# Optimization experiments

Hardware: AMD Instinct MI355X
Metric: run time of the kernel (lower is better)

Reference implementation:

```python
import jax, jax.numpy as jnp
import numpy as np

B, S, L, H, D = 32, 512, 8, 1024, 64  # batch, max seq len, max span, hidden, MLP width


def setup_inputs() -> dict:
    key = jax.random.key(0)
    ks = jax.random.split(key, 8)
    return {
        "hidden": jax.random.normal(ks[0], (B, S, H), jnp.float32),
        "seq_lengths": jax.random.randint(ks[1], (B,), S // 2, S + 1),
        "term_weight": jax.random.normal(ks[2], (H,), jnp.float32),
        "W1": jax.random.normal(ks[3], (H, D), jnp.float32) * 0.02,
        "b1": jnp.zeros((D,), jnp.float32),
        "W2": jax.random.normal(ks[4], (D, 1), jnp.float32) * 0.02,
        "b2": jnp.zeros((1,), jnp.float32),
        "Ws": jax.random.normal(ks[5], (H, 1), jnp.float32) * 0.02,
        "bs": jnp.zeros((1,), jnp.float32),
    }


def reference(hidden, seq_lengths, term_weight, W1, b1, W2, b2, Ws, bs):
    """Batched candidate-span TermAttention + span scoring.

    For each sentence b (true length seq_lengths[b]) and start s, spans of
    nominal length l+1 (l in 0..L-1) cover positions s..s+l clipped to the
    sentence end, exactly as get_candidate_span_pairs/get_span_hiddens.
    TermAttention: softmax over MLP((h * w)) within the span, weighted sum,
    then spanEmb2Score linear -> scalar per span.
    """
    Bn, Sn, Hn = hidden.shape
    j = jnp.arange(L)
    s = jnp.arange(Sn)
    pos = jnp.minimum(s[:, None] + j[None, :], Sn - 1)          # [S,L] clipped gather idx
    g = hidden[:, pos]                                           # [B,S,L,H] span positions
    # per-position attention logit (independent of span length)
    e = (jax.nn.relu((g * term_weight) @ W1 + b1) @ W2 + b2)[..., 0]  # [B,S,L]
    # valid_pos[b,s,jp]: position s+jp is inside sentence b
    valid_pos = (s[:, None] + j[None, :])[None] < seq_lengths[:, None, None]  # [B,S,L]
    # m[b,s,l,jp]: position jp belongs to span of length l+1 and is in-sentence
    tri = j[:, None] >= j[None, :]                               # [L,L] jp <= l
    m = valid_pos[:, :, None, :] & tri[None, None]               # [B,S,L,L]
    logits = jnp.where(m, e[:, :, None, :], -1e9)
    a = jax.nn.softmax(logits, axis=-1) * m                      # [B,S,L,L]
    emb = jnp.einsum('bslj,bsjh->bslh', a, g)                    # span embeddings
    scores = (emb @ Ws + bs)[..., 0]                             # [B,S,L]
    valid_span = s[None, :, None] < seq_lengths[:, None, None]
    return jnp.where(valid_span, scores, 0.0)
```

## Files before the change

kernel.cpp:

```cpp
#include <hip/hip_runtime.h>
#include <hip/hip_bf16.h>

#define BB 32
#define SS 512
#define LL 8
#define HH 1024
#define DD 64

#define BM 32
#define BK 32
#define APAD 40

typedef __attribute__((ext_vector_type(8))) short bf16x8;
typedef __attribute__((ext_vector_type(4))) float f32x4;

__device__ __forceinline__ unsigned short f2bf(float x) {
    unsigned int u = __float_as_uint(x);
    u += 0x7FFFu + ((u >> 16) & 1u);
    return (unsigned short)(u >> 16);
}

__global__ void k_prep(const float* __restrict__ W1,
                       const float* __restrict__ tw,
                       unsigned short* __restrict__ W1pT) {
    int i = blockIdx.x * 256 + threadIdx.x;
    int h = i >> 6;
    int d = i & 63;
    float val = tw[h] * W1[i];
    W1pT[d * HH + h] = f2bf(val);
}

__global__ __launch_bounds__(256) void k_main(
        const float* __restrict__ hidden,
        const unsigned short* __restrict__ W1pT,
        const float* __restrict__ b1,
        const float* __restrict__ W2,
        const float* __restrict__ b2,
        const float* __restrict__ Ws,
        float* __restrict__ e1,
        float* __restrict__ vout) {
    __shared__ unsigned short Alds[BM * APAD];
    __shared__ unsigned short Blds[DD * APAD];
    __shared__ float eplds[4][BM];

    const int tid = threadIdx.x;
    const int row0 = blockIdx.x * BM;

    const int ln   = tid & 63;
    const int wv   = tid >> 6;
    const int ln15 = ln & 15;
    const int quad = ln >> 4;

    const int ar  = tid >> 3;
    const int ako = (tid & 7) * 4;
    const int bd  = tid >> 2;
    const int bko = (tid & 3) * 8;

    f32x4 acc0 = {0.f, 0.f, 0.f, 0.f};
    f32x4 acc1 = {0.f, 0.f, 0.f, 0.f};
    float vp = 0.f;

    const float* arow = hidden + (size_t)(row0 + ar) * HH + ako;
    const unsigned short* brow = W1pT + (size_t)bd * HH + bko;

    for (int k0 = 0; k0 < HH; k0 += BK) {
        float4 h4 = *(const float4*)(arow + k0);
        float4 w4 = *(const float4*)(Ws + k0 + ako);
        vp += h4.x * w4.x + h4.y * w4.y + h4.z * w4.z + h4.w * w4.w;
        ushort4 a4;
        a4.x = f2bf(h4.x); a4.y = f2bf(h4.y); a4.z = f2bf(h4.z); a4.w = f2bf(h4.w);
        *(ushort4*)&Alds[ar * APAD + ako] = a4;
        *(uint4*)&Blds[bd * APAD + bko] = *(const uint4*)(brow + k0);
        __syncthreads();

        bf16x8 bfrag = *(const bf16x8*)&Blds[(wv * 16 + ln15) * APAD + quad * 8];
        bf16x8 af0   = *(const bf16x8*)&Alds[(ln15) * APAD + quad * 8];
        bf16x8 af1   = *(const bf16x8*)&Alds[(16 + ln15) * APAD + quad * 8];
        acc0 = __builtin_amdgcn_mfma_f32_16x16x32_bf16(af0, bfrag, acc0, 0, 0, 0);
        acc1 = __builtin_amdgcn_mfma_f32_16x16x32_bf16(af1, bfrag, acc1, 0, 0, 0);
        __syncthreads();
    }

    vp += __shfl_xor(vp, 1);
    vp += __shfl_xor(vp, 2);
    vp += __shfl_xor(vp, 4);
    if ((tid & 7) == 0) vout[row0 + (tid >> 3)] = vp;

    const int col = wv * 16 + ln15;
    const float b1c = b1[col];
    const float w2c = W2[col];
    float ep[8];
#pragma unroll
    for (int reg = 0; reg < 4; reg++) {
        float x0 = acc0[reg] + b1c;
        float x1 = acc1[reg] + b1c;
        ep[reg]     = fmaxf(x0, 0.f) * w2c;
        ep[4 + reg] = fmaxf(x1, 0.f) * w2c;
    }
#pragma unroll
    for (int off = 1; off < 16; off <<= 1) {
#pragma unroll
        for (int i = 0; i < 8; i++) ep[i] += __shfl_xor(ep[i], off);
    }
    if (ln15 == 0) {
#pragma unroll
        for (int reg = 0; reg < 4; reg++) {
            eplds[wv][quad * 4 + reg]      = ep[reg];
            eplds[wv][16 + quad * 4 + reg] = ep[4 + reg];
        }
    }
    __syncthreads();
    if (tid < BM) {
        float e = b2[0] + eplds[0][tid] + eplds[1][tid] + eplds[2][tid] + eplds[3][tid];
        e1[row0 + tid] = e;
    }
}

__global__ __launch_bounds__(256) void k_span(
        const float* __restrict__ e1,
        const float* __restrict__ v,
        const int* __restrict__ seq_lengths,
        const float* __restrict__ bs,
        float* __restrict__ out) {
    int i = blockIdx.x * 256 + threadIdx.x;
    int b = i >> 9;
    int s = i & (SS - 1);
    int sl = seq_lengths[b];
    float res[LL];

    if (s >= sl) {
#pragma unroll
        for (int l = 0; l < LL; l++) res[l] = 0.f;
    } else {
        const float bsv = bs[0];
        float e[LL], vv[LL];
        int base = b << 9;
#pragma unroll
        for (int j = 0; j < LL; j++) {
            int pos = s + j; if (pos > SS - 1) pos = SS - 1;
            e[j]  = e1[base + pos];
            vv[j] = v[base + pos];
        }
        float M = e[0], Z = 1.f, W = vv[0];
        res[0] = W / Z + bsv;
#pragma unroll
        for (int l = 1; l < LL; l++) {
            if (s + l < sl) {
                float el = e[l];
                if (el > M) {
                    float c = __expf(M - el);
                    Z = Z * c + 1.f;
                    W = W * c + vv[l];
                    M = el;
                } else {
                    float p = __expf(el - M);
                    Z += p;
                    W += p * vv[l];
                }
            }
            res[l] = W / Z + bsv;
        }
    }
    float4* o = (float4*)(out + (size_t)i * LL);
    o[0] = make_float4(res[0], res[1], res[2], res[3]);
    o[1] = make_float4(res[4], res[5], res[6], res[7]);
}

extern "C" void kernel_launch(void* const* d_in, const int* in_sizes, int n_in,
                              void* d_out, int out_size, void* d_ws, size_t ws_size,
                              hipStream_t stream) {
    const float* hidden = (const float*)d_in[0];
    const int*   seqlen = (const int*)d_in[1];
    const float* tw     = (const float*)d_in[2];
    const float* W1     = (const float*)d_in[3];
    const float* b1     = (const float*)d_in[4];
    const float* W2     = (const float*)d_in[5];
    const float* b2     = (const float*)d_in[6];
    const float* Ws     = (const float*)d_in[7];
    const float* bs     = (const float*)d_in[8];
    float* out = (float*)d_out;

    unsigned short* W1pT = (unsigned short*)d_ws;
    float* e1 = (float*)((char*)d_ws + 131072);
    float* vv = (float*)((char*)d_ws + 131072 + 65536);

    k_prep<<<(HH * DD) / 256, 256, 0, stream>>>(W1, tw, W1pT);

    k_main<<<(BB * SS) / BM, 256, 0, stream>>>(hidden, W1pT, b1, W2, b2, Ws, e1, vv);

    k_span<<<(BB * SS) / 256, 256, 0, stream>>>(e1, vv, seqlen, bs, out);
}
```

Before: 134.5 us.

## Stage full 16-row A tile in LDS and stream W1 fragments from global

The main GEMM kernel now uses 16-row blocks and loads each block's full 16x1024 hidden tile into LDS once, converting it to bf16 and computing the Ws dot product in that same pass. The K loop then runs 32 unrolled MFMAs with no barriers, reading B fragments straight from global memory (L2-resident W1pT) instead of staging them through LDS. This removes the two barriers per K step and doubles the block count for better occupancy and latency hiding. In exchange, each block rereads the whole W1pT from cache and uses about 33 KB of LDS per block.

```diff
diff --git a/kernel.cpp b/kernel.cpp
--- a/kernel.cpp
+++ b/kernel.cpp
@@ -7,9 +7,8 @@
 #define HH 1024
 #define DD 64
 
-#define BM 32
-#define BK 32
-#define APAD 40
+#define BM 16
+#define ROWSTR 1032
 
 typedef __attribute__((ext_vector_type(8))) short bf16x8;
 typedef __attribute__((ext_vector_type(4))) float f32x4;
@@ -39,80 +38,70 @@
         const float* __restrict__ Ws,
         float* __restrict__ e1,
         float* __restrict__ vout) {
-    __shared__ unsigned short Alds[BM * APAD];
-    __shared__ unsigned short Blds[DD * APAD];
+    __shared__ unsigned short Alds[BM * ROWSTR];
     __shared__ float eplds[4][BM];
 
     const int tid = threadIdx.x;
     const int row0 = blockIdx.x * BM;
 
+    {
+        const int r  = tid >> 4;
+        const int co = (tid & 15) * 4;
+        const float* arow = hidden + (size_t)(row0 + r) * HH + co;
+        float vp = 0.f;
+#pragma unroll
+        for (int i = 0; i < 16; i++) {
+            float4 h4 = *(const float4*)(arow + i * 64);
+            float4 w4 = *(const float4*)(Ws + co + i * 64);
+            vp += h4.x * w4.x + h4.y * w4.y + h4.z * w4.z + h4.w * w4.w;
+            ushort4 a4;
+            a4.x = f2bf(h4.x); a4.y = f2bf(h4.y); a4.z = f2bf(h4.z); a4.w = f2bf(h4.w);
+            *(ushort4*)&Alds[r * ROWSTR + co + i * 64] = a4;
+        }
+        vp += __shfl_xor(vp, 1);
+        vp += __shfl_xor(vp, 2);
+        vp += __shfl_xor(vp, 4);
+        vp += __shfl_xor(vp, 8);
+        if ((tid & 15) == 0) vout[row0 + r] = vp;
+    }
+    __syncthreads();
+
+    const int wv   = tid >> 6;
     const int ln   = tid & 63;
-    const int wv   = tid >> 6;
     const int ln15 = ln & 15;
     const int quad = ln >> 4;
 
-    const int ar  = tid >> 3;
-    const int ako = (tid & 7) * 4;
-    const int bd  = tid >> 2;
-    const int bko = (tid & 3) * 8;
+    const unsigned short* bptr = W1pT + (size_t)(wv * 16 + ln15) * HH + quad * 8;
+    const unsigned short* aptr = &Alds[ln15 * ROWSTR + quad * 8];
 
-    f32x4 acc0 = {0.f, 0.f, 0.f, 0.f};
-    f32x4 acc1 = {0.f, 0.f, 0.f, 0.f};
-    float vp = 0.f;
-
-    const float* arow = hidden + (size_t)(row0 + ar) * HH + ako;
-    const unsigned short* brow = W1pT + (size_t)bd * HH + bko;
-
-    for (int k0 = 0; k0 < HH; k0 += BK) {
-        float4 h4 = *(const float4*)(arow + k0);
-        float4 w4 = *(const float4*)(Ws + k0 + ako);
-        vp += h4.x * w4.x + h4.y * w4.y + h4.z * w4.z + h4.w * w4.w;
-        ushort4 a4;
-        a4.x = f2bf(h4.x); a4.y = f2bf(h4.y); a4.z = f2bf(h4.z); a4.w = f2bf(h4.w);
-        *(ushort4*)&Alds[ar * APAD + ako] = a4;
-        *(uint4*)&Blds[bd * APAD + bko] = *(const uint4*)(brow + k0);
-        __syncthreads();
-
-        bf16x8 bfrag = *(const bf16x8*)&Blds[(wv * 16 + ln15) * APAD + quad * 8];
-        bf16x8 af0   = *(const bf16x8*)&Alds[(ln15) * APAD + quad * 8];
-        bf16x8 af1   = *(const bf16x8*)&Alds[(16 + ln15) * APAD + quad * 8];
-        acc0 = __builtin_amdgcn_mfma_f32_16x16x32_bf16(af0, bfrag, acc0, 0, 0, 0);
-        acc1 = __builtin_amdgcn_mfma_f32_16x16x32_bf16(af1, bfrag, acc1, 0, 0, 0);
-        __syncthreads();
+    f32x4 acc = {0.f, 0.f, 0.f, 0.f};
+#pragma unroll
+    for (int c = 0; c < 32; c++) {
+        bf16x8 bfrag = *(const bf16x8*)(bptr + c * 32);
+        bf16x8 afrag = *(const bf16x8*)(aptr + c * 32);
+        acc = __builtin_amdgcn_mfma_f32_16x16x32_bf16(afrag, bfrag, acc, 0, 0, 0);
     }
-
-    vp += __shfl_xor(vp, 1);
-    vp += __shfl_xor(vp, 2);
-    vp += __shfl_xor(vp, 4);
-    if ((tid & 7) == 0) vout[row0 + (tid >> 3)] = vp;
 
     const int col = wv * 16 + ln15;
     const float b1c = b1[col];
     const float w2c = W2[col];
-    float ep[8];
+    float ep[4];
 #pragma unroll
     for (int reg = 0; reg < 4; reg++) {
-        float x0 = acc0[reg] + b1c;
-        float x1 = acc1[reg] + b1c;
-        ep[reg]     = fmaxf(x0, 0.f) * w2c;
-        ep[4 + reg] = fmaxf(x1, 0.f) * w2c;
+        ep[reg] = fmaxf(acc[reg] + b1c, 0.f) * w2c;
     }
 #pragma unroll
     for (int off = 1; off < 16; off <<= 1) {
 #pragma unroll
-        for (int i = 0; i < 8; i++) ep[i] += __shfl_xor(ep[i], off);
+        for (int i = 0; i < 4; i++) ep[i] += __shfl_xor(ep[i], off);
     }
     if (ln15 == 0) {
 #pragma unroll
-        for (int reg = 0; reg < 4; reg++) {
-            eplds[wv][quad * 4 + reg]      = ep[reg];
-            eplds[wv][16 + quad * 4 + reg] = ep[4 + reg];
-        }
+        for (int reg = 0; reg < 4; reg++) eplds[wv][quad * 4 + reg] = ep[reg];
     }
     __syncthreads();
     if (tid < BM) {
-        float e = b2[0] + eplds[0][tid] + eplds[1][tid] + eplds[2][tid] + eplds[3][tid];
-        e1[row0 + tid] = e;
+        e1[row0 + tid] = b2[0] + eplds[0][tid] + eplds[1][tid] + eplds[2][tid] + eplds[3][tid];
     }
 }
 
```

After: 124.8 us. 1.08x faster.
